# Optimization experiments

Measured on AMD Instinct MI355X. Metric: run time of the kernel, lower is better.

Reference implementation:

```python
import jax, jax.numpy as jnp
import numpy as np

B, N, C, HF, WF, D = 2, 6, 64, 112, 200, 64
BEV_H, BEV_W = 200, 200


def _view_matrix(h, w, h_m=100.0, w_m=100.0, offset=0.0):
    sh, sw = h / h_m, w / w_m
    return np.array([[0.0, -sw, w / 2.0],
                     [-sh, 0.0, h * offset + h / 2.0],
                     [0.0, 0.0, 1.0]], dtype=np.float32)


def setup_inputs() -> dict:
    key = jax.random.key(0)
    k1, k2 = jax.random.split(key)
    feat_bn = jax.random.normal(k1, (B * N, C, HF, WF), jnp.float32)
    depth_prob = jax.nn.softmax(jax.random.normal(k2, (B * N, D, HF, WF), jnp.float32), axis=1)
    # structured inverse intrinsics (pinhole, f = W/2)
    f = 0.5 * WF
    K = np.array([[f, 0.0, WF / 2.0], [0.0, f, HF / 2.0], [0.0, 0.0, 1.0]], np.float32)
    I_inv = np.broadcast_to(np.linalg.inv(K).astype(np.float32), (B, N, 3, 3)).copy()
    # random rigid cam->ego extrinsics inverse: orthonormal rotation + translation, cam height 1.5m
    rng = np.random.default_rng(0)
    E_inv = np.tile(np.eye(4, dtype=np.float32), (B, N, 1, 1))
    for bi in range(B):
        for ni in range(N):
            Q, _ = np.linalg.qr(rng.normal(size=(3, 3)))
            E_inv[bi, ni, :3, :3] = Q.astype(np.float32)
            E_inv[bi, ni, :3, 3] = np.array([rng.uniform(-2, 2), rng.uniform(-2, 2), 1.5], np.float32)
    V = jnp.asarray(_view_matrix(BEV_H, BEV_W))
    feat_hw = jnp.array([HF, WF], jnp.int32)
    return {"feat_bn": feat_bn, "depth_prob": depth_prob, "I_inv": jnp.asarray(I_inv),
            "E_inv": jnp.asarray(E_inv), "V": V, "feat_hw": feat_hw, "n": N}


def reference(feat_bn, depth_prob, I_inv, E_inv, V, feat_hw, n):
    bn, Cc, h, w = feat_bn.shape
    b = bn // n
    hw = h * w
    HW = BEV_H * BEV_W
    dt = feat_bn.dtype

    # pixel grid; source does rearrange('d w h -> d (h w)') on an [3,h,w] tensor,
    # i.e. flattens with the *width* axis outer -> transpose before reshape (bug-faithful).
    u, v = jnp.meshgrid(jnp.arange(w, dtype=dt), jnp.arange(h, dtype=dt))  # each [h, w]
    pix = jnp.stack([u, v, jnp.ones_like(u)], 0)          # [3, h, w]
    pix = pix.transpose(0, 2, 1).reshape(3, hw)           # [3, hw]

    I_inv_bn = I_inv.reshape(bn, 3, 3)
    E_inv_bn = E_inv.reshape(bn, 4, 4)
    cam = jnp.einsum('bij,jp->bip', I_inv_bn, pix)        # [bn, 3, hw]
    cam = jnp.concatenate([cam, jnp.ones((bn, 1, hw), dt)], axis=1)  # pad homogeneous 1
    d = jnp.einsum('bij,bjp->bip', E_inv_bn, cam).transpose(0, 2, 1)[..., :3]  # [bn, hw, 3]
    c = E_inv_bn[:, :3, 3][:, None, :]                    # [bn, 1, 3] camera center

    # ray-ground intersection (z = 0 plane)
    s = -c[..., 2] / jnp.maximum(d[..., 2], 1e-6)
    xy_ego = c[..., :2] + d[..., :2] * s[..., None]       # [bn, hw, 2]

    # ego -> BEV pixel coords via view matrix V
    homo = jnp.concatenate([xy_ego, jnp.ones_like(xy_ego[..., :1])], axis=-1)
    proj = homo @ V.T
    bev_xy = proj[..., :2] / jnp.maximum(proj[..., 2:], 1e-7)

    gx = bev_xy[..., 0] / (BEV_W - 1) * 2 - 1
    gy = bev_xy[..., 1] / (BEV_H - 1) * 2 - 1
    conf = depth_prob.max(axis=1).reshape(bn, hw)          # [bn, hw]

    px = (gx + 1) * (BEV_W - 1) / 2
    py = (gy + 1) * (BEV_H - 1) / 2
    x0 = jnp.clip(jnp.floor(px), 0, BEV_W - 1)
    y0 = jnp.clip(jnp.floor(py), 0, BEV_H - 1)
    x1 = jnp.clip(x0 + 1, 0, BEV_W - 1)
    y1 = jnp.clip(y0 + 1, 0, BEV_H - 1)

    corners = [(x0, y0, (x1 - px) * (y1 - py)),
               (x1, y0, (px - x0) * (y1 - py)),
               (x0, y1, (x1 - px) * (py - y0)),
               (x1, y1, (px - x0) * (py - y0))]

    idx = jnp.concatenate([y.astype(jnp.int32) * BEV_W + x.astype(jnp.int32)
                           for x, y, _ in corners], axis=1)             # [bn, 4hw]
    wgt = jnp.concatenate([wg * conf for _, _, wg in corners], axis=1)  # [bn, 4hw]

    feat_flat = feat_bn.reshape(bn, Cc, hw)
    wfeat = jnp.tile(feat_flat, (1, 1, 4)) * wgt[:, None, :]            # [bn, C, 4hw]

    idx_flat = (idx + jnp.arange(bn, dtype=jnp.int32)[:, None] * HW).reshape(-1)
    vals = wfeat.transpose(0, 2, 1).reshape(-1, Cc)                      # [bn*4hw, C]
    bev = jax.ops.segment_sum(vals, idx_flat, num_segments=bn * HW)      # [bn*HW, C]
    bev = bev.reshape(b, n, HW, Cc).transpose(0, 1, 3, 2).reshape(b, n, Cc, BEV_H, BEV_W)
    return bev.mean(axis=1)
```

## Files before the change

### kernel.cpp

```cpp
#include <hip/hip_runtime.h>
#include <hip/hip_fp16.h>

#define BB   2
#define NN   6
#define CCH  64
#define HFE  112
#define WFE  200
#define DDE  64
#define HWF  (HFE*WFE)
#define HWF4 (HWF/4)
#define BEVH 200
#define BEVW 200
#define HWB  (BEVH*BEVW)
#define NBINS (BB*HWB)
#define NBINS_PAD 81920
#define NSCANB (NBINS_PAD/256)
#define MAXENT1 (BB*NN*HWF)
#define NCHUNK1 (MAXENT1/64)
#define ACC_ELEMS ((size_t)BB*HWB*CCH)

__device__ __forceinline__ float4 f4max(float4 a, float4 b) {
    return make_float4(fmaxf(a.x,b.x), fmaxf(a.y,b.y), fmaxf(a.z,b.z), fmaxf(a.w,b.w));
}

__device__ __forceinline__ uint4 pack8h(float4 a, float4 b) {
    __half2 h0 = __float22half2_rn(make_float2(a.x, a.y));
    __half2 h1 = __float22half2_rn(make_float2(a.z, a.w));
    __half2 h2 = __float22half2_rn(make_float2(b.x, b.y));
    __half2 h3 = __float22half2_rn(make_float2(b.z, b.w));
    uint4 u;
    u.x = *(unsigned*)&h0; u.y = *(unsigned*)&h1;
    u.z = *(unsigned*)&h2; u.w = *(unsigned*)&h3;
    return u;
}

struct Geo {
    int valid;
    int c00, c10, c01, c11;
    float w00, w10, w01, w11;
};

__device__ __forceinline__ Geo geo_compute(int bn, int p,
    const float* __restrict__ I_inv, const float* __restrict__ E_inv,
    const float* __restrict__ Vm)
{
    Geo g; g.valid = 0;
    const float u = (float)(p / HFE);
    const float v = (float)(p % HFE);
    const float* Ii = I_inv + bn * 9;
    const float* Ei = E_inv + bn * 16;
    float cx = Ii[0]*u + Ii[1]*v + Ii[2];
    float cy = Ii[3]*u + Ii[4]*v + Ii[5];
    float cz = Ii[6]*u + Ii[7]*v + Ii[8];
    float tx = Ei[3], ty = Ei[7], tz = Ei[11];
    float dx = Ei[0]*cx + Ei[1]*cy + Ei[2] *cz + tx;
    float dy = Ei[4]*cx + Ei[5]*cy + Ei[6] *cz + ty;
    float dz = Ei[8]*cx + Ei[9]*cy + Ei[10]*cz + tz;
    float s  = -tz / fmaxf(dz, 1e-6f);
    float ex = tx + dx * s;
    float ey = ty + dy * s;
    float prx = Vm[0]*ex + Vm[1]*ey + Vm[2];
    float pry = Vm[3]*ex + Vm[4]*ey + Vm[5];
    float prz = Vm[6]*ex + Vm[7]*ey + Vm[8];
    float den = fmaxf(prz, 1e-7f);
    float bx = prx / den, by = pry / den;
    float gx = bx / (float)(BEVW-1) * 2.0f - 1.0f;
    float gy = by / (float)(BEVH-1) * 2.0f - 1.0f;
    float px = (gx + 1.0f) * (float)(BEVW-1) / 2.0f;
    float py = (gy + 1.0f) * (float)(BEVH-1) / 2.0f;
    float x0f = fminf(fmaxf(floorf(px), 0.0f), (float)(BEVW-1));
    float y0f = fminf(fmaxf(floorf(py), 0.0f), (float)(BEVH-1));
    float x1f = fminf(x0f + 1.0f, (float)(BEVW-1));
    float y1f = fminf(y0f + 1.0f, (float)(BEVH-1));
    if (x0f == x1f || y0f == y1f) return g;
    float wx0 = x1f - px, wx1 = px - x0f;
    float wy0 = y1f - py, wy1 = py - y0f;
    int x0 = (int)x0f, x1 = (int)x1f, y0 = (int)y0f, y1 = (int)y1f;
    g.c00 = y0*BEVW + x0;  g.w00 = wx0*wy0;
    g.c10 = y0*BEVW + x1;  g.w10 = wx1*wy0;
    g.c01 = y1*BEVW + x0;  g.w01 = wx0*wy1;
    g.c11 = y1*BEVW + x1;  g.w11 = wx1*wy1;
    g.valid = 1;
    return g;
}

__device__ __forceinline__ void run_info(int cell, int lane,
                                         bool& leader, int& runlen, int& leadlane)
{
    int prev = __shfl_up(cell, 1);
    bool change = (lane == 0) || (cell != prev);
    unsigned long long bal = __ballot(change);
    unsigned long long below = bal & (~0ull >> (63 - lane));
    leadlane = 63 - __builtin_clzll(below);
    unsigned long long above = (lane == 63) ? 0ull : (bal >> (lane + 1));
    int next = (above == 0ull) ? 64 : (lane + 1 + __builtin_ffsll((long long)above) - 1);
    runlen = next - lane;
    leader = change && (cell >= 0);
}

__device__ __forceinline__ unsigned pack2w(float a, float b) {
    unsigned ua = __float2uint_rn(a * 65535.0f);
    unsigned ub = __float2uint_rn(b * 65535.0f);
    return ua | (ub << 16);
}

__global__ __launch_bounds__(256) void transpose_kernel(
    const float* __restrict__ feat,
    __half* __restrict__ feat_t)
{
    __shared__ float tile[4][16][68];

    const int bn   = blockIdx.y;
    const int p0   = blockIdx.x * 64;
    const int tid  = threadIdx.x;
    const int lane = tid & 63, wv = tid >> 6;
    const int lq   = lane & 3;
    const int lh   = lane >> 2;
    const int pw   = p0 + 16 * wv;

    const float* fcam = feat + (size_t)bn * CCH * HWF;
    float4 f[4];
#pragma unroll
    for (int i = 0; i < 4; ++i)
        f[i] = *(const float4*)(fcam + (size_t)(16*i + lh) * HWF + pw + 4*lq);

#pragma unroll
    for (int i = 0; i < 4; ++i) {
        tile[wv][4*lq + 0][16*i + lh] = f[i].x;
        tile[wv][4*lq + 1][16*i + lh] = f[i].y;
        tile[wv][4*lq + 2][16*i + lh] = f[i].z;
        tile[wv][4*lq + 3][16*i + lh] = f[i].w;
    }

    __half* ocam = feat_t + (size_t)bn * HWF * CCH;
#pragma unroll
    for (int s = 0; s < 2; ++s) {
        const int row = 8*s + (lane >> 3);
        const int c0  = 8 * (lane & 7);
        float4 a = *(const float4*)(&tile[wv][row][c0]);
        float4 b = *(const float4*)(&tile[wv][row][c0 + 4]);
        uint4 u = pack8h(a, b);
        *(uint4*)(ocam + (size_t)(pw + row) * CCH + c0) = u;
    }
}

__global__ __launch_bounds__(256) void conf_hist_kernel(
    const float* __restrict__ depth,
    const float* __restrict__ I_inv, const float* __restrict__ E_inv,
    const float* __restrict__ Vm,
    float* __restrict__ conf,
    int* __restrict__ counts)
{
    const int bn   = blockIdx.y;
    const int p0   = blockIdx.x * 128;
    const int tid  = threadIdx.x;
    const int lane = tid & 63, wv = tid >> 6;
    const int lq   = lane & 3;
    const int lh   = lane >> 2;
    const int pw   = p0 + 32 * wv;

    const float* dcam = depth + (size_t)bn * DDE * HWF;
    float4 d0[4], d1[4];
#pragma unroll
    for (int i = 0; i < 4; ++i)
        d0[i] = *(const float4*)(dcam + (size_t)(lh + 16*i) * HWF + pw + 4*lq);
#pragma unroll
    for (int i = 0; i < 4; ++i)
        d1[i] = *(const float4*)(dcam + (size_t)(lh + 16*i) * HWF + pw + 16 + 4*lq);

    float4 m0 = f4max(f4max(d0[0], d0[1]), f4max(d0[2], d0[3]));
    float4 m1 = f4max(f4max(d1[0], d1[1]), f4max(d1[2], d1[3]));
#pragma unroll
    for (int m = 4; m <= 32; m <<= 1) {
        m0.x = fmaxf(m0.x, __shfl_xor(m0.x, m));
        m0.y = fmaxf(m0.y, __shfl_xor(m0.y, m));
        m0.z = fmaxf(m0.z, __shfl_xor(m0.z, m));
        m0.w = fmaxf(m0.w, __shfl_xor(m0.w, m));
        m1.x = fmaxf(m1.x, __shfl_xor(m1.x, m));
        m1.y = fmaxf(m1.y, __shfl_xor(m1.y, m));
        m1.z = fmaxf(m1.z, __shfl_xor(m1.z, m));
        m1.w = fmaxf(m1.w, __shfl_xor(m1.w, m));
    }
    if (lh == 0) {
        *(float4*)(conf + (size_t)bn * HWF + pw + 4*lq)      = m0;
        *(float4*)(conf + (size_t)bn * HWF + pw + 16 + 4*lq) = m1;
    }

    {
        Geo g = geo_compute(bn, pw + (lane & 31), I_inv, E_inv, Vm);
        const int base = (bn / NN) * HWB;
        const int cell = ((lane < 32) && g.valid) ? base + g.c00 : -1;
        bool leader; int runlen, leadlane;
        run_info(cell, lane, leader, runlen, leadlane);
        if (leader) atomicAdd(&counts[cell], runlen);
    }
}

__global__ __launch_bounds__(256) void scan1_kernel(
    const int* __restrict__ counts, int* __restrict__ offsets, int* __restrict__ bsum)
{
    __shared__ int tmp[256];
    const int t = threadIdx.x;
    const int i = blockIdx.x * 256 + t;
    int v = counts[i];
    tmp[t] = v; __syncthreads();
    for (int off = 1; off < 256; off <<= 1) {
        int x = (t >= off) ? tmp[t - off] : 0;
        __syncthreads();
        tmp[t] += x;
        __syncthreads();
    }
    offsets[i] = tmp[t] - v;
    if (t == 255) bsum[blockIdx.x] = tmp[255];
}

__global__ __launch_bounds__(256) void scan3_kernel(
    int* __restrict__ offsets, const int* __restrict__ bsum, int* __restrict__ cursor)
{
    __shared__ int s[256];
    const int t = threadIdx.x;
    int part = 0;
    for (int i = t; i < blockIdx.x; i += 256) part += bsum[i];
    s[t] = part; __syncthreads();
    for (int off = 128; off > 0; off >>= 1) {
        if (t < off) s[t] += s[t + off];
        __syncthreads();
    }
    const int i = blockIdx.x * 256 + t;
    int v = offsets[i] + s[0];
    offsets[i] = v;
    cursor[i]  = v;
}

__global__ __launch_bounds__(256) void place_kernel(
    const float* __restrict__ conf,
    const float* __restrict__ I_inv, const float* __restrict__ E_inv,
    const float* __restrict__ Vm,
    int* __restrict__ cursor, uint4* __restrict__ entries)
{
    const int bn = blockIdx.y;
    const int p  = blockIdx.x * blockDim.x + threadIdx.x;
    const int lane = threadIdx.x & 63;
    const int inb = (p < HWF);
    const int pp = inb ? p : HWF - 1;
    Geo g = geo_compute(bn, pp, I_inv, E_inv, Vm);
    const int valid = inb && g.valid;
    if (__ballot(valid) == 0ull) return;
    const int base = (bn / NN) * HWB;
    const int bin  = valid ? base + g.c00 : -1;

    bool leader; int runlen, leadlane;
    run_info(bin, lane, leader, runlen, leadlane);
    int pos_leader = 0;
    if (leader) pos_leader = atomicAdd(&cursor[bin], runlen);
    int pos = __shfl(pos_leader, leadlane) + (lane - leadlane);
    if (valid) {
        const float cf = conf[(size_t)bn * HWF + pp];
        entries[pos] = make_uint4((unsigned)bin, (unsigned)(bn * HWF + pp),
                                  pack2w(g.w00 * cf, g.w10 * cf),
                                  pack2w(g.w01 * cf, g.w11 * cf));
    }
}

__global__ __launch_bounds__(256) void gather_seg_kernel(
    const uint4* __restrict__ entries, const int* __restrict__ total_ptr,
    const __half* __restrict__ feat_t, float* __restrict__ acc)
{
    const int lane = threadIdx.x & 63, wv = threadIdx.x >> 6;
    const int chunk = blockIdx.x * 4 + wv;
    const int total = *total_ptr;
    const int start = chunk * 64;
    if (start >= total) return;
    const int m = min(64, total - start);

    const float inv = 1.0f / 65535.0f;
    float a00 = 0.f, a10 = 0.f, a01 = 0.f, a11 = 0.f;

    int j = 0;
    for (; j + 8 <= m; j += 8) {
        uint4 ent[8];
#pragma unroll
        for (int k = 0; k < 8; ++k) ent[k] = entries[start + j + k];
        const unsigned nextbin = (j + 8 < m) ? entries[start + j + 8].x : 0xFFFFFFFFu;
        float f[8];
#pragma unroll
        for (int k = 0; k < 8; ++k)
            f[k] = __half2float(feat_t[(size_t)ent[k].y * CCH + lane]);
#pragma unroll
        for (int k = 0; k < 8; ++k) {
            a00 = fmaf(f[k], (float)(ent[k].z & 0xffffu) * inv, a00);
            a10 = fmaf(f[k], (float)(ent[k].z >> 16)     * inv, a10);
            a01 = fmaf(f[k], (float)(ent[k].w & 0xffffu) * inv, a01);
            a11 = fmaf(f[k], (float)(ent[k].w >> 16)     * inv, a11);
            const unsigned nb = (k < 7) ? ent[k + 1].x : nextbin;
            if (ent[k].x != nb) {
                float* ab = acc + (size_t)ent[k].x * CCH + lane;
                atomicAdd(ab,                     a00);
                atomicAdd(ab + (size_t)1   * CCH, a10);
                atomicAdd(ab + (size_t)200 * CCH, a01);
                atomicAdd(ab + (size_t)201 * CCH, a11);
                a00 = a10 = a01 = a11 = 0.f;
            }
        }
    }
    for (; j < m; ++j) {
        uint4 e = entries[start + j];
        float fv = __half2float(feat_t[(size_t)e.y * CCH + lane]);
        a00 = fmaf(fv, (float)(e.z & 0xffffu) * inv, a00);
        a10 = fmaf(fv, (float)(e.z >> 16)     * inv, a10);
        a01 = fmaf(fv, (float)(e.w & 0xffffu) * inv, a01);
        a11 = fmaf(fv, (float)(e.w >> 16)     * inv, a11);
        const unsigned nb = (j + 1 < m) ? entries[start + j + 1].x : 0xFFFFFFFFu;
        if (e.x != nb) {
            float* ab = acc + (size_t)e.x * CCH + lane;
            atomicAdd(ab,                     a00);
            atomicAdd(ab + (size_t)1   * CCH, a10);
            atomicAdd(ab + (size_t)200 * CCH, a01);
            atomicAdd(ab + (size_t)201 * CCH, a11);
            a00 = a10 = a01 = a11 = 0.f;
        }
    }
}

__global__ __launch_bounds__(256) void finalize_kernel(
    const float* __restrict__ acc, float* __restrict__ out)
{
    __shared__ float t[64][66];
    const int b     = blockIdx.y;
    const int cell0 = blockIdx.x * 64;
    const int cc    = threadIdx.x >> 2;
    const int q     = threadIdx.x & 3;

    const float* abase = acc + ((size_t)b * HWB + cell0) * CCH;
#pragma unroll
    for (int i = 0; i < 4; ++i) {
        const int cg = q + 4 * i;
        float4 f = *(const float4*)(abase + (size_t)cc * CCH + 4 * cg);
        t[cc][4*cg+0] = f.x; t[cc][4*cg+1] = f.y;
        t[cc][4*cg+2] = f.z; t[cc][4*cg+3] = f.w;
    }
    __syncthreads();
    float* obase = out + (size_t)b * CCH * HWB + cell0;
#pragma unroll
    for (int i = 0; i < 4; ++i) {
        const int lg = q + 4 * i;
        float4 o;
        o.x = t[4*lg+0][cc] * (1.0f/6.0f);
        o.y = t[4*lg+1][cc] * (1.0f/6.0f);
        o.z = t[4*lg+2][cc] * (1.0f/6.0f);
        o.w = t[4*lg+3][cc] * (1.0f/6.0f);
        *(float4*)(obase + (size_t)cc * HWB + 4 * lg) = o;
    }
}

__global__ __launch_bounds__(256) void splat_kernel(
    const float* __restrict__ feat, const float* __restrict__ depth,
    const float* __restrict__ I_inv, const float* __restrict__ E_inv,
    const float* __restrict__ Vm, float* __restrict__ acc)
{
    __shared__ float fshare[64][65];
    __shared__ float cpart2[4][64];
    const int bn = blockIdx.y, b = bn / NN, p0 = blockIdx.x * 64;
    const int lane = threadIdx.x & 63, wv = threadIdx.x >> 6;
    const float* fbase = feat + (size_t)bn * CCH * HWF + p0;
#pragma unroll
    for (int c = wv; c < CCH; c += 4)
        fshare[lane][c] = fbase[(size_t)c * HWF + lane];
    const float* dbase = depth + (size_t)bn * DDE * HWF + p0;
    float m = dbase[(size_t)(wv * 16) * HWF + lane];
#pragma unroll
    for (int d = wv * 16 + 1; d < wv * 16 + 16; ++d)
        m = fmaxf(m, dbase[(size_t)d * HWF + lane]);
    cpart2[wv][lane] = m;
    __syncthreads();
    float* ab = acc + ((size_t)b * HWB) * CCH + lane;
    for (int s = wv * 16; s < wv * 16 + 16; ++s) {
        Geo g = geo_compute(bn, p0 + s, I_inv, E_inv, Vm);
        if (!g.valid) continue;
        float cf = fmaxf(fmaxf(cpart2[0][s], cpart2[1][s]), fmaxf(cpart2[2][s], cpart2[3][s]));
        float f = fshare[s][lane];
        atomicAdd(ab + (size_t)g.c00 * CCH, f * (g.w00 * cf));
        atomicAdd(ab + (size_t)g.c10 * CCH, f * (g.w10 * cf));
        atomicAdd(ab + (size_t)g.c01 * CCH, f * (g.w01 * cf));
        atomicAdd(ab + (size_t)g.c11 * CCH, f * (g.w11 * cf));
    }
}

extern "C" void kernel_launch(void* const* d_in, const int* in_sizes, int n_in,
                              void* d_out, int out_size, void* d_ws, size_t ws_size,
                              hipStream_t stream) {
    const float* feat  = (const float*)d_in[0];
    const float* depth = (const float*)d_in[1];
    const float* I_inv = (const float*)d_in[2];
    const float* E_inv = (const float*)d_in[3];
    const float* Vm    = (const float*)d_in[4];
    float* out = (float*)d_out;

    size_t off = 0;
    char* wsb = (char*)d_ws;
    auto carve = [&](size_t bytes) -> void* {
        void* p = wsb + off; off += (bytes + 255) & ~(size_t)255; return p;
    };
    __half* feat_t = (__half*)carve((size_t)BB * NN * CCH * HWF * 2);
    float* acc     = (float*)carve(ACC_ELEMS * 4);
    int*   counts  = (int*)  carve((NBINS_PAD + 256) * 4);
    uint4* entries = (uint4*)carve((size_t)MAXENT1 * 16);
    float* conf    = (float*)carve((size_t)BB * NN * HWF * 4);
    int*   offsets = (int*)  carve((NBINS_PAD + 256) * 4);
    int*   cursor  = (int*)  carve((NBINS_PAD + 256) * 4);
    int*   bsum    = (int*)  carve(NSCANB * 4);

    if (off <= ws_size) {
        hipMemsetAsync(acc, 0, ACC_ELEMS * 4 + (NBINS_PAD + 256) * 4, stream);

        dim3 tgrid(HWF / 64, BB * NN);
        transpose_kernel<<<tgrid, 256, 0, stream>>>(feat, feat_t);

        dim3 cgrid(HWF / 128, BB * NN);
        conf_hist_kernel<<<cgrid, 256, 0, stream>>>(depth, I_inv, E_inv, Vm,
                                                    conf, counts);

        scan1_kernel<<<NSCANB, 256, 0, stream>>>(counts, offsets, bsum);
        scan3_kernel<<<NSCANB, 256, 0, stream>>>(offsets, bsum, cursor);

        dim3 plgrid((HWF + 255) / 256, BB * NN);
        place_kernel<<<plgrid, 256, 0, stream>>>(conf, I_inv, E_inv, Vm,
                                                 cursor, entries);

        gather_seg_kernel<<<NCHUNK1 / 4, 256, 0, stream>>>(
            entries, offsets + NBINS, feat_t, acc);

        dim3 fgrid(HWB / 64, BB);
        finalize_kernel<<<fgrid, 256, 0, stream>>>(acc, out);
    } else {
        float* acc0 = (float*)d_ws;
        hipMemsetAsync(acc0, 0, ACC_ELEMS * 4, stream);
        dim3 grid(HWF / 64, BB * NN);
        splat_kernel<<<grid, 256, 0, stream>>>(feat, depth, I_inv, E_inv, Vm, acc0);
        dim3 fgrid(HWB / 64, BB);
        finalize_kernel<<<fgrid, 256, 0, stream>>>(acc0, out);
    }
}
```

Measured before the change: 254.7 us.

## Fuse all stages into one cooperative persistent kernel with grid syncs

Replaces the memset plus seven separate launches (transpose, conf/histogram, two scans, place, gather, finalize) with one cooperative kernel that zeroes buffers, fuses transpose with the depth-max confidence pass, and separates phases with grid-wide syncs. The aim is to remove per-launch overhead and the idle gaps between small kernels. The fused first phase also reads depth with fewer loads per tile. The cost is grid.sync barriers, a persistent grid sized from occupancy, and possible register pressure from the large fused kernel. The old splat fallback is removed.

```diff
diff --git a/kernel.cpp b/kernel.cpp
--- a/kernel.cpp
+++ b/kernel.cpp
@@ -1,5 +1,8 @@
 #include <hip/hip_runtime.h>
 #include <hip/hip_fp16.h>
+#include <hip/hip_cooperative_groups.h>
+
+namespace cg = cooperative_groups;
 
 #define BB   2
 #define NN   6
@@ -8,7 +11,6 @@
 #define WFE  200
 #define DDE  64
 #define HWF  (HFE*WFE)
-#define HWF4 (HWF/4)
 #define BEVH 200
 #define BEVW 200
 #define HWB  (BEVH*BEVW)
@@ -36,7 +38,7 @@
 
 struct Geo {
     int valid;
-    int c00, c10, c01, c11;
+    int c00;
     float w00, w10, w01, w11;
 };
 
@@ -44,7 +46,8 @@
     const float* __restrict__ I_inv, const float* __restrict__ E_inv,
     const float* __restrict__ Vm)
 {
-    Geo g; g.valid = 0;
+    Geo g; g.valid = 0; g.c00 = -1;
+    g.w00 = g.w10 = g.w01 = g.w11 = 0.f;
     const float u = (float)(p / HFE);
     const float v = (float)(p % HFE);
     const float* Ii = I_inv + bn * 9;
@@ -75,11 +78,10 @@
     if (x0f == x1f || y0f == y1f) return g;
     float wx0 = x1f - px, wx1 = px - x0f;
     float wy0 = y1f - py, wy1 = py - y0f;
-    int x0 = (int)x0f, x1 = (int)x1f, y0 = (int)y0f, y1 = (int)y1f;
-    g.c00 = y0*BEVW + x0;  g.w00 = wx0*wy0;
-    g.c10 = y0*BEVW + x1;  g.w10 = wx1*wy0;
-    g.c01 = y1*BEVW + x0;  g.w01 = wx0*wy1;
-    g.c11 = y1*BEVW + x1;  g.w11 = wx1*wy1;
+    int x0 = (int)x0f, y0 = (int)y0f;
+    g.c00 = y0*BEVW + x0;
+    g.w00 = wx0*wy0;  g.w10 = wx1*wy0;
+    g.w01 = wx0*wy1;  g.w11 = wx1*wy1;
     g.valid = 1;
     return g;
 }
@@ -104,12 +106,251 @@
     return ua | (ub << 16);
 }
 
+__global__ __launch_bounds__(256) void mega_kernel(
+    const float* __restrict__ feat, const float* __restrict__ depth,
+    const float* __restrict__ I_inv, const float* __restrict__ E_inv,
+    const float* __restrict__ Vm,
+    __half* __restrict__ feat_t, float* __restrict__ conf,
+    int* __restrict__ counts, int* __restrict__ offsets, int* __restrict__ cursor,
+    int* __restrict__ bsum, uint4* __restrict__ entries,
+    float* __restrict__ acc, float* __restrict__ out)
+{
+    cg::grid_group grid = cg::this_grid();
+    __shared__ __align__(16) unsigned char smem[17408];
+
+    const int tid  = threadIdx.x;
+    const int lane = tid & 63, wv = tid >> 6;
+    const int bid  = blockIdx.x, nb = gridDim.x;
+
+    {
+        float4* a4 = (float4*)acc;
+        const int n4 = (int)(ACC_ELEMS / 4);
+        for (int i = bid * 256 + tid; i < n4; i += nb * 256)
+            a4[i] = make_float4(0.f, 0.f, 0.f, 0.f);
+        for (int i = bid * 256 + tid; i < NBINS_PAD + 256; i += nb * 256)
+            counts[i] = 0;
+    }
+    grid.sync();
+
+    {
+        float (*tile)[16][68] = (float (*)[16][68])(void*)smem;
+        const int lq = lane & 3;
+        const int lh = lane >> 2;
+        for (int t = bid; t < 350 * (BB * NN); t += nb) {
+            const int bn = t / 350;
+            const int p0 = (t % 350) * 64;
+            const int pw = p0 + 16 * wv;
+
+            const float* fcam = feat + (size_t)bn * CCH * HWF;
+            float4 f[4];
+#pragma unroll
+            for (int i = 0; i < 4; ++i)
+                f[i] = *(const float4*)(fcam + (size_t)(16*i + lh) * HWF + pw + 4*lq);
+
+            const float* dcam = depth + (size_t)bn * DDE * HWF;
+            float4 mx;
+            {
+                float4 d0 = *(const float4*)(dcam + (size_t)(lh     ) * HWF + pw + 4*lq);
+                float4 d1 = *(const float4*)(dcam + (size_t)(lh + 16) * HWF + pw + 4*lq);
+                float4 d2 = *(const float4*)(dcam + (size_t)(lh + 32) * HWF + pw + 4*lq);
+                float4 d3 = *(const float4*)(dcam + (size_t)(lh + 48) * HWF + pw + 4*lq);
+                mx = f4max(f4max(d0, d1), f4max(d2, d3));
+            }
+
+#pragma unroll
+            for (int i = 0; i < 4; ++i) {
+                tile[wv][4*lq + 0][16*i + lh] = f[i].x;
+                tile[wv][4*lq + 1][16*i + lh] = f[i].y;
+                tile[wv][4*lq + 2][16*i + lh] = f[i].z;
+                tile[wv][4*lq + 3][16*i + lh] = f[i].w;
+            }
+
+#pragma unroll
+            for (int m = 4; m <= 32; m <<= 1) {
+                mx.x = fmaxf(mx.x, __shfl_xor(mx.x, m));
+                mx.y = fmaxf(mx.y, __shfl_xor(mx.y, m));
+                mx.z = fmaxf(mx.z, __shfl_xor(mx.z, m));
+                mx.w = fmaxf(mx.w, __shfl_xor(mx.w, m));
+            }
+            if (lh == 0)
+                *(float4*)(conf + (size_t)bn * HWF + pw + 4*lq) = mx;
+
+            __half* ocam = feat_t + (size_t)bn * HWF * CCH;
+#pragma unroll
+            for (int s = 0; s < 2; ++s) {
+                const int row = 8*s + (lane >> 3);
+                const int c0  = 8 * (lane & 7);
+                float4 a = *(const float4*)(&tile[wv][row][c0]);
+                float4 b = *(const float4*)(&tile[wv][row][c0 + 4]);
+                uint4 u = pack8h(a, b);
+                *(uint4*)(ocam + (size_t)(pw + row) * CCH + c0) = u;
+            }
+
+            if (wv == 0) {
+                Geo g = geo_compute(bn, p0 + lane, I_inv, E_inv, Vm);
+                const int base = (bn / NN) * HWB;
+                const int cell = g.valid ? base + g.c00 : -1;
+                bool leader; int runlen, leadlane;
+                run_info(cell, lane, leader, runlen, leadlane);
+                if (leader) atomicAdd(&counts[cell], runlen);
+            }
+        }
+    }
+    grid.sync();
+
+    if (bid < NSCANB) {
+        int* tmp = (int*)(void*)smem;
+        const int i = bid * 256 + tid;
+        int v = counts[i];
+        tmp[tid] = v; __syncthreads();
+        for (int off = 1; off < 256; off <<= 1) {
+            int x = (tid >= off) ? tmp[tid - off] : 0;
+            __syncthreads();
+            tmp[tid] += x;
+            __syncthreads();
+        }
+        offsets[i] = tmp[tid] - v;
+        if (tid == 255) bsum[bid] = tmp[255];
+    }
+    grid.sync();
+
+    if (bid < NSCANB) {
+        int* s = (int*)(void*)smem;
+        int part = 0;
+        for (int i = tid; i < bid; i += 256) part += bsum[i];
+        s[tid] = part; __syncthreads();
+        for (int off = 128; off > 0; off >>= 1) {
+            if (tid < off) s[tid] += s[tid + off];
+            __syncthreads();
+        }
+        const int i = bid * 256 + tid;
+        int v = offsets[i] + s[0];
+        offsets[i] = v;
+        cursor[i]  = v;
+    }
+    grid.sync();
+
+    {
+        for (int t = bid; t < 88 * (BB * NN); t += nb) {
+            const int bn = t / 88;
+            const int p  = (t % 88) * 256 + tid;
+            const int inb = (p < HWF);
+            const int pp = inb ? p : HWF - 1;
+            Geo g = geo_compute(bn, pp, I_inv, E_inv, Vm);
+            const int valid = inb && g.valid;
+            if (__ballot(valid) == 0ull) continue;
+            const int base = (bn / NN) * HWB;
+            const int bin  = valid ? base + g.c00 : -1;
+
+            bool leader; int runlen, leadlane;
+            run_info(bin, lane, leader, runlen, leadlane);
+            int pos_leader = 0;
+            if (leader) pos_leader = atomicAdd(&cursor[bin], runlen);
+            int pos = __shfl(pos_leader, leadlane) + (lane - leadlane);
+            if (valid) {
+                const float cf = conf[(size_t)bn * HWF + pp];
+                entries[pos] = make_uint4((unsigned)bin, (unsigned)(bn * HWF + pp),
+                                          pack2w(g.w00 * cf, g.w10 * cf),
+                                          pack2w(g.w01 * cf, g.w11 * cf));
+            }
+        }
+    }
+    grid.sync();
+
+    {
+        const int total = offsets[NBINS];
+        const float inv = 1.0f / 65535.0f;
+        for (int gb = bid; gb < NCHUNK1 / 4; gb += nb) {
+            const int chunk = gb * 4 + wv;
+            const int start = chunk * 64;
+            if (start >= total) continue;
+            const int m = min(64, total - start);
+
+            float a00 = 0.f, a10 = 0.f, a01 = 0.f, a11 = 0.f;
+            int j = 0;
+            for (; j + 8 <= m; j += 8) {
+                uint4 ent[8];
+#pragma unroll
+                for (int k = 0; k < 8; ++k) ent[k] = entries[start + j + k];
+                const unsigned nextbin = (j + 8 < m) ? entries[start + j + 8].x : 0xFFFFFFFFu;
+                float f[8];
+#pragma unroll
+                for (int k = 0; k < 8; ++k)
+                    f[k] = __half2float(feat_t[(size_t)ent[k].y * CCH + lane]);
+#pragma unroll
+                for (int k = 0; k < 8; ++k) {
+                    a00 = fmaf(f[k], (float)(ent[k].z & 0xffffu) * inv, a00);
+                    a10 = fmaf(f[k], (float)(ent[k].z >> 16)     * inv, a10);
+                    a01 = fmaf(f[k], (float)(ent[k].w & 0xffffu) * inv, a01);
+                    a11 = fmaf(f[k], (float)(ent[k].w >> 16)     * inv, a11);
+                    const unsigned nbn = (k < 7) ? ent[k + 1].x : nextbin;
+                    if (ent[k].x != nbn) {
+                        float* ab = acc + (size_t)ent[k].x * CCH + lane;
+                        atomicAdd(ab,                     a00);
+                        atomicAdd(ab + (size_t)1   * CCH, a10);
+                        atomicAdd(ab + (size_t)200 * CCH, a01);
+                        atomicAdd(ab + (size_t)201 * CCH, a11);
+                        a00 = a10 = a01 = a11 = 0.f;
+                    }
+                }
+            }
+            for (; j < m; ++j) {
+                uint4 e = entries[start + j];
+                float fv = __half2float(feat_t[(size_t)e.y * CCH + lane]);
+                a00 = fmaf(fv, (float)(e.z & 0xffffu) * inv, a00);
+                a10 = fmaf(fv, (float)(e.z >> 16)     * inv, a10);
+                a01 = fmaf(fv, (float)(e.w & 0xffffu) * inv, a01);
+                a11 = fmaf(fv, (float)(e.w >> 16)     * inv, a11);
+                const unsigned nbn = (j + 1 < m) ? entries[start + j + 1].x : 0xFFFFFFFFu;
+                if (e.x != nbn) {
+                    float* ab = acc + (size_t)e.x * CCH + lane;
+                    atomicAdd(ab,                     a00);
+                    atomicAdd(ab + (size_t)1   * CCH, a10);
+                    atomicAdd(ab + (size_t)200 * CCH, a01);
+                    atomicAdd(ab + (size_t)201 * CCH, a11);
+                    a00 = a10 = a01 = a11 = 0.f;
+                }
+            }
+        }
+    }
+    grid.sync();
+
+    {
+        float (*tt)[66] = (float (*)[66])(void*)smem;
+        const int cc = tid >> 2;
+        const int q  = tid & 3;
+        for (int t = bid; t < 2 * 625; t += nb) {
+            const int b     = t / 625;
+            const int cell0 = (t % 625) * 64;
+            __syncthreads();
+            const float* abase = acc + ((size_t)b * HWB + cell0) * CCH;
+#pragma unroll
+            for (int i = 0; i < 4; ++i) {
+                const int cg = q + 4 * i;
+                float4 f = *(const float4*)(abase + (size_t)cc * CCH + 4 * cg);
+                tt[cc][4*cg+0] = f.x; tt[cc][4*cg+1] = f.y;
+                tt[cc][4*cg+2] = f.z; tt[cc][4*cg+3] = f.w;
+            }
+            __syncthreads();
+            float* obase = out + (size_t)b * CCH * HWB + cell0;
+#pragma unroll
+            for (int i = 0; i < 4; ++i) {
+                const int lg = q + 4 * i;
+                float4 o;
+                o.x = tt[4*lg+0][cc] * (1.0f/6.0f);
+                o.y = tt[4*lg+1][cc] * (1.0f/6.0f);
+                o.z = tt[4*lg+2][cc] * (1.0f/6.0f);
+                o.w = tt[4*lg+3][cc] * (1.0f/6.0f);
+                *(float4*)(obase + (size_t)cc * HWB + 4 * lg) = o;
+            }
+        }
+    }
+}
+
 __global__ __launch_bounds__(256) void transpose_kernel(
-    const float* __restrict__ feat,
-    __half* __restrict__ feat_t)
+    const float* __restrict__ feat, __half* __restrict__ feat_t)
 {
     __shared__ float tile[4][16][68];
-
     const int bn   = blockIdx.y;
     const int p0   = blockIdx.x * 64;
     const int tid  = threadIdx.x;
@@ -123,7 +364,6 @@
 #pragma unroll
     for (int i = 0; i < 4; ++i)
         f[i] = *(const float4*)(fcam + (size_t)(16*i + lh) * HWF + pw + 4*lq);
-
 #pragma unroll
     for (int i = 0; i < 4; ++i) {
         tile[wv][4*lq + 0][16*i + lh] = f[i].x;
@@ -131,7 +371,6 @@
         tile[wv][4*lq + 2][16*i + lh] = f[i].z;
         tile[wv][4*lq + 3][16*i + lh] = f[i].w;
     }
-
     __half* ocam = feat_t + (size_t)bn * HWF * CCH;
 #pragma unroll
     for (int s = 0; s < 2; ++s) {
@@ -148,8 +387,7 @@
     const float* __restrict__ depth,
     const float* __restrict__ I_inv, const float* __restrict__ E_inv,
     const float* __restrict__ Vm,
-    float* __restrict__ conf,
-    int* __restrict__ counts)
+    float* __restrict__ conf, int* __restrict__ counts)
 {
     const int bn   = blockIdx.y;
     const int p0   = blockIdx.x * 128;
@@ -185,7 +423,6 @@
         *(float4*)(conf + (size_t)bn * HWF + pw + 4*lq)      = m0;
         *(float4*)(conf + (size_t)bn * HWF + pw + 16 + 4*lq) = m1;
     }
-
     {
         Geo g = geo_compute(bn, pw + (lane & 31), I_inv, E_inv, Vm);
         const int base = (bn / NN) * HWB;
@@ -275,7 +512,6 @@
 
     const float inv = 1.0f / 65535.0f;
     float a00 = 0.f, a10 = 0.f, a01 = 0.f, a11 = 0.f;
-
     int j = 0;
     for (; j + 8 <= m; j += 8) {
         uint4 ent[8];
@@ -292,8 +528,8 @@
             a10 = fmaf(f[k], (float)(ent[k].z >> 16)     * inv, a10);
             a01 = fmaf(f[k], (float)(ent[k].w & 0xffffu) * inv, a01);
             a11 = fmaf(f[k], (float)(ent[k].w >> 16)     * inv, a11);
-            const unsigned nb = (k < 7) ? ent[k + 1].x : nextbin;
-            if (ent[k].x != nb) {
+            const unsigned nbn = (k < 7) ? ent[k + 1].x : nextbin;
+            if (ent[k].x != nbn) {
                 float* ab = acc + (size_t)ent[k].x * CCH + lane;
                 atomicAdd(ab,                     a00);
                 atomicAdd(ab + (size_t)1   * CCH, a10);
@@ -310,8 +546,8 @@
         a10 = fmaf(fv, (float)(e.z >> 16)     * inv, a10);
         a01 = fmaf(fv, (float)(e.w & 0xffffu) * inv, a01);
         a11 = fmaf(fv, (float)(e.w >> 16)     * inv, a11);
-        const unsigned nb = (j + 1 < m) ? entries[start + j + 1].x : 0xFFFFFFFFu;
-        if (e.x != nb) {
+        const unsigned nbn = (j + 1 < m) ? entries[start + j + 1].x : 0xFFFFFFFFu;
+        if (e.x != nbn) {
             float* ab = acc + (size_t)e.x * CCH + lane;
             atomicAdd(ab,                     a00);
             atomicAdd(ab + (size_t)1   * CCH, a10);
@@ -350,39 +586,6 @@
         o.z = t[4*lg+2][cc] * (1.0f/6.0f);
         o.w = t[4*lg+3][cc] * (1.0f/6.0f);
         *(float4*)(obase + (size_t)cc * HWB + 4 * lg) = o;
-    }
-}
-
-__global__ __launch_bounds__(256) void splat_kernel(
-    const float* __restrict__ feat, const float* __restrict__ depth,
-    const float* __restrict__ I_inv, const float* __restrict__ E_inv,
-    const float* __restrict__ Vm, float* __restrict__ acc)
-{
-    __shared__ float fshare[64][65];
-    __shared__ float cpart2[4][64];
-    const int bn = blockIdx.y, b = bn / NN, p0 = blockIdx.x * 64;
-    const int lane = threadIdx.x & 63, wv = threadIdx.x >> 6;
-    const float* fbase = feat + (size_t)bn * CCH * HWF + p0;
-#pragma unroll
-    for (int c = wv; c < CCH; c += 4)
-        fshare[lane][c] = fbase[(size_t)c * HWF + lane];
-    const float* dbase = depth + (size_t)bn * DDE * HWF + p0;
-    float m = dbase[(size_t)(wv * 16) * HWF + lane];
-#pragma unroll
-    for (int d = wv * 16 + 1; d < wv * 16 + 16; ++d)
-        m = fmaxf(m, dbase[(size_t)d * HWF + lane]);
-    cpart2[wv][lane] = m;
-    __syncthreads();
-    float* ab = acc + ((size_t)b * HWB) * CCH + lane;
-    for (int s = wv * 16; s < wv * 16 + 16; ++s) {
-        Geo g = geo_compute(bn, p0 + s, I_inv, E_inv, Vm);
-        if (!g.valid) continue;
-        float cf = fmaxf(fmaxf(cpart2[0][s], cpart2[1][s]), fmaxf(cpart2[2][s], cpart2[3][s]));
-        float f = fshare[s][lane];
-        atomicAdd(ab + (size_t)g.c00 * CCH, f * (g.w00 * cf));
-        atomicAdd(ab + (size_t)g.c10 * CCH, f * (g.w10 * cf));
-        atomicAdd(ab + (size_t)g.c01 * CCH, f * (g.w01 * cf));
-        atomicAdd(ab + (size_t)g.c11 * CCH, f * (g.w11 * cf));
     }
 }
 
@@ -409,8 +612,39 @@
     int*   offsets = (int*)  carve((NBINS_PAD + 256) * 4);
     int*   cursor  = (int*)  carve((NBINS_PAD + 256) * 4);
     int*   bsum    = (int*)  carve(NSCANB * 4);
-
-    if (off <= ws_size) {
+    (void)ws_size;
+
+    static int s_grid = -2;
+    if (s_grid == -2) {
+        int dev = 0;
+        hipGetDevice(&dev);
+        hipDeviceProp_t prop;
+        if (hipGetDeviceProperties(&prop, dev) == hipSuccess && prop.cooperativeLaunch) {
+            int maxb = 0;
+            if (hipOccupancyMaxActiveBlocksPerMultiprocessor(&maxb, mega_kernel, 256, 0)
+                    == hipSuccess && maxb > 0) {
+                long g = (long)maxb * prop.multiProcessorCount;
+                if (g > 2048) g = 2048;
+                s_grid = (int)g;
+            } else s_grid = 0;
+        } else s_grid = 0;
+    }
+
+    bool done = false;
+    if (s_grid >= 64) {
+        void* kargs[14] = {
+            (void*)&feat, (void*)&depth, (void*)&I_inv, (void*)&E_inv, (void*)&Vm,
+            (void*)&feat_t, (void*)&conf, (void*)&counts, (void*)&offsets,
+            (void*)&cursor, (void*)&bsum, (void*)&entries, (void*)&acc, (void*)&out
+        };
+        hipError_t err = hipLaunchCooperativeKernel(mega_kernel,
+                                                    dim3((unsigned)s_grid), dim3(256),
+                                                    kargs, 0, stream);
+        if (err == hipSuccess) done = true;
+        else s_grid = 0;
+    }
+
+    if (!done) {
         hipMemsetAsync(acc, 0, ACC_ELEMS * 4 + (NBINS_PAD + 256) * 4, stream);
 
         dim3 tgrid(HWF / 64, BB * NN);
@@ -432,12 +666,5 @@
 
         dim3 fgrid(HWB / 64, BB);
         finalize_kernel<<<fgrid, 256, 0, stream>>>(acc, out);
-    } else {
-        float* acc0 = (float*)d_ws;
-        hipMemsetAsync(acc0, 0, ACC_ELEMS * 4, stream);
-        dim3 grid(HWF / 64, BB * NN);
-        splat_kernel<<<grid, 256, 0, stream>>>(feat, depth, I_inv, E_inv, Vm, acc0);
-        dim3 fgrid(HWB / 64, BB);
-        finalize_kernel<<<fgrid, 256, 0, stream>>>(acc0, out);
-    }
-}
+    }
+}
```

Result: slower. 708.6 us (+178.3%).
